# Performance work log

Hardware: AMD Instinct MI355X
Metric: run time of the kernel (lower is better)

Reference implementation:

```python
import jax, jax.numpy as jnp
import numpy as np

N = 12288
IN_DIM = 256
OUT_DIM = 128
NEG_SLOPE = 0.01  # torch nn.LeakyReLU default


def setup_inputs() -> dict:
    key = jax.random.key(0)
    k1, k2, k3, k4, k5 = jax.random.split(key, 5)
    adj_mx = jax.random.randint(k1, (N, N), 0, 2, dtype=jnp.int32)
    input_features = jax.random.normal(k2, (N, IN_DIM), dtype=jnp.float32)
    # Linear(in_dim, out_dim): weight [out, in], bias [out]
    W = jax.random.normal(k3, (OUT_DIM, IN_DIM), dtype=jnp.float32) / np.sqrt(IN_DIM)
    b = jax.random.normal(k4, (OUT_DIM,), dtype=jnp.float32) * 0.01
    phi = jax.random.normal(k5, (2 * OUT_DIM, 1), dtype=jnp.float32)
    return {"adj_mx": adj_mx, "input_features": input_features, "W": W, "b": b, "phi": phi}


def reference(adj_mx, input_features, W, b, phi):
    # projection (dropout is identity in eval): [N, out]
    new_features = input_features @ W.T + b
    # additive attention halves: (N,1) + (1,N) -> [N,N]
    first_half = new_features @ phi[:OUT_DIM]          # [N,1]
    second_half = (new_features @ phi[OUT_DIM:]).T     # [1,N]
    similarity = jax.nn.leaky_relu(first_half + second_half, NEG_SLOPE)
    # adjacency with self-loops; mask non-edges to -1e20
    adj_hat = adj_mx.astype(jnp.float32) + jnp.eye(adj_mx.shape[0], dtype=jnp.float32)
    masked = jnp.where(adj_hat > 0, similarity, jnp.float32(-1e20))
    att = jax.nn.softmax(masked, axis=1)               # row-wise softmax [N,N]
    out = att @ new_features                           # [N, out]
    return jax.nn.leaky_relu(out, NEG_SLOPE)
```

## Files before the change

kernel.cpp:

```cpp
#include <hip/hip_runtime.h>
#include <hip/hip_bf16.h>

#define N_NODES 12288
#define IN_DIM 256
#define OUT_DIM 128
#define NEG 0.01f
#define LOG2E 1.44269504088896340736f
#define NSPLIT 16
#define JSPAN (N_NODES / NSPLIT)
#define TJ 64
#define NT (JSPAN / TJ)

typedef __attribute__((ext_vector_type(8))) short short8;
typedef __attribute__((ext_vector_type(4))) float f32x4;
typedef __attribute__((ext_vector_type(4))) int i32x4;

__device__ __forceinline__ float fast_exp2(float x) {
#if __has_builtin(__builtin_amdgcn_exp2f)
  return __builtin_amdgcn_exp2f(x);
#else
  return exp2f(x);
#endif
}

__device__ __forceinline__ unsigned short f2bf(float x) {
  unsigned u = __float_as_uint(x);
  unsigned r = (u + 0x7FFFu + ((u >> 16) & 1u)) >> 16;
  return (unsigned short)r;
}

__global__ __launch_bounds__(256) void k1_proj(
    const float* __restrict__ X, const float* __restrict__ W,
    const float* __restrict__ bias, const float* __restrict__ phi,
    unsigned short* __restrict__ Vt, float* __restrict__ f,
    float* __restrict__ s, unsigned* __restrict__ smax) {
  __shared__ float Xs[32][40];
  __shared__ float Ws[32][136];
  __shared__ unsigned skey[8];
  const int t = threadIdx.x;
  const int i0 = blockIdx.x * 32;
  const int tx = t & 31, ty = t >> 5;
  float acc[4][4] = {};
  for (int k0 = 0; k0 < IN_DIM; k0 += 32) {
    __syncthreads();
    {
      int r = t >> 3, kq = (t & 7) * 4;
      float4 xv = *(const float4*)&X[(size_t)(i0 + r) * IN_DIM + k0 + kq];
      Xs[kq + 0][r] = xv.x; Xs[kq + 1][r] = xv.y;
      Xs[kq + 2][r] = xv.z; Xs[kq + 3][r] = xv.w;
    }
#pragma unroll
    for (int q = 0; q < 4; ++q) {
      int idx = t + q * 256;
      int c = idx >> 3, kq = (idx & 7) * 4;
      float4 wv = *(const float4*)&W[(size_t)c * IN_DIM + k0 + kq];
      Ws[kq + 0][c] = wv.x; Ws[kq + 1][c] = wv.y;
      Ws[kq + 2][c] = wv.z; Ws[kq + 3][c] = wv.w;
    }
    __syncthreads();
#pragma unroll
    for (int kk = 0; kk < 32; ++kk) {
      float4 a = *(const float4*)&Xs[kk][ty * 4];
      float4 bv = *(const float4*)&Ws[kk][tx * 4];
      float av[4] = {a.x, a.y, a.z, a.w};
      float bw[4] = {bv.x, bv.y, bv.z, bv.w};
#pragma unroll
      for (int r = 0; r < 4; ++r)
#pragma unroll
        for (int c = 0; c < 4; ++c) acc[r][c] += av[r] * bw[c];
    }
  }
  float4 bv = *(const float4*)&bias[tx * 4];
  float bb[4] = {bv.x, bv.y, bv.z, bv.w};
  float4 p1 = *(const float4*)&phi[tx * 4];
  float4 p2 = *(const float4*)&phi[OUT_DIM + tx * 4];
  float p1a[4] = {p1.x, p1.y, p1.z, p1.w};
  float p2a[4] = {p2.x, p2.y, p2.z, p2.w};
  float fp[4], sp_[4];
#pragma unroll
  for (int r = 0; r < 4; ++r) {
    int i = i0 + ty * 4 + r;
    float o[4];
    fp[r] = 0.f; sp_[r] = 0.f;
#pragma unroll
    for (int c = 0; c < 4; ++c) {
      o[c] = acc[r][c] + bb[c];
      Vt[(size_t)(tx * 4 + c) * N_NODES + i] = f2bf(o[c]);
      fp[r] = __builtin_fmaf(o[c], p1a[c], fp[r]);
      sp_[r] = __builtin_fmaf(o[c], p2a[c], sp_[r]);
    }
  }
#pragma unroll
  for (int o = 16; o; o >>= 1) {
#pragma unroll
    for (int r = 0; r < 4; ++r) {
      fp[r] += __shfl_xor(fp[r], o);
      sp_[r] += __shfl_xor(sp_[r], o);
    }
  }
  if (tx == 0) {
    unsigned kmax = 0;
#pragma unroll
    for (int r = 0; r < 4; ++r) {
      int i = i0 + ty * 4 + r;
      f[i] = fp[r]; s[i] = sp_[r];
      unsigned u = __float_as_uint(sp_[r]);
      unsigned key = (u & 0x80000000u) ? ~u : (u | 0x80000000u);
      kmax = max(kmax, key);
    }
    skey[ty] = kmax;
  }
  __syncthreads();
  if (t == 0) {
    unsigned kmax = skey[0];
#pragma unroll
    for (int q = 1; q < 8; ++q) kmax = max(kmax, skey[q]);
    atomicMax(smax, kmax);
  }
}

__global__ __launch_bounds__(256) void k3_attn(
    const int* __restrict__ adj, const unsigned short* __restrict__ Vt,
    const float* __restrict__ f, const float* __restrict__ s,
    const unsigned* __restrict__ smaxk,
    float* __restrict__ pacc, float* __restrict__ pden) {
  __shared__ float s_lds[JSPAN];
  __shared__ __align__(16) unsigned short vbuf[2][128 * TJ];
  const int t = threadIdx.x;
  const int sp = blockIdx.x & (NSPLIT - 1);
  const int rb = blockIdx.x >> 4;
  const int j0g = sp * JSPAN;
  const int w = t >> 6, l = t & 63;
  const int m = l & 15, slot = l >> 4;
  const int row_g = rb * 64 + w * 16 + m;
  if (t < JSPAN / 4) {
    *(float4*)&s_lds[t * 4] = *(const float4*)&s[j0g + t * 4];
  }
  unsigned key = *smaxk;
  unsigned ku = (key & 0x80000000u) ? (key ^ 0x80000000u) : ~key;
  const float smaxv = __uint_as_float(ku);
  const float fi = f[row_g];
  const float xm = fi + smaxv;
  const float mrow = fmaxf(xm, NEG * xm);
  const float em = mrow * LOG2E;
  const int diag_g = row_g - j0g;
  float dsum = 0.f;
  f32x4 acc[8] = {};
  const int* adjp = adj + (size_t)row_g * N_NODES + j0g + 8 * slot;
  const int srow = t >> 3, schunk = t & 7;
  const int xsw = schunk ^ (srow & 7);
  const unsigned short* vt_src = Vt + (size_t)srow * N_NODES + j0g + xsw * 8;
  const int off0 = m * TJ + ((slot) ^ (m & 7)) * 8;
  const int off1 = m * TJ + ((4 + slot) ^ (m & 7)) * 8;
  i32x4 aA[4], aB[4];

#define ADJ_LOAD(SET, TT) { int _o = (TT) * TJ;                       \
    SET[0] = *(const i32x4*)(adjp + _o);                              \
    SET[1] = *(const i32x4*)(adjp + _o + 4);                          \
    SET[2] = *(const i32x4*)(adjp + _o + 32);                         \
    SET[3] = *(const i32x4*)(adjp + _o + 36); }

#define STAGE(BB, TT) { const unsigned short* _s = vt_src + (TT) * TJ;      \
    unsigned short* _d = &vbuf[BB][t * 8];                                  \
    __builtin_amdgcn_global_load_lds(_s,                    _d,        16, 0, 0); \
    __builtin_amdgcn_global_load_lds(_s + 32 * N_NODES,     _d + 2048, 16, 0, 0); \
    __builtin_amdgcn_global_load_lds(_s + 64 * N_NODES,     _d + 4096, 16, 0, 0); \
    __builtin_amdgcn_global_load_lds(_s + 96 * N_NODES,     _d + 6144, 16, 0, 0); }

  STAGE(0, 0);
  ADJ_LOAD(aA, 0);
  ADJ_LOAD(aB, 1);

#define ITER(TT, SET) {                                                     \
    __syncthreads();      \
    STAGE(((TT) + 1) & 1, ((TT) + 1 < NT) ? (TT) + 1 : NT - 1);             \
    const unsigned short* rdp = &vbuf[(TT) & 1][0];                         \
    short8 b0[8], b1[8];                                                    \
    _Pragma("unroll")                                                       \
    for (int nt = 0; nt < 8; ++nt)                                          \
      b0[nt] = *(const short8*)(rdp + off0 + nt * 16 * TJ);                 \
    _Pragma("unroll")                                                       \
    for (int nt = 0; nt < 8; ++nt)                                          \
      b1[nt] = *(const short8*)(rdp + off1 + nt * 16 * TJ);                 \
    short8 af0, af1;                                                        \
    _Pragma("unroll")                                                       \
    for (int c = 0; c < 2; ++c) {                                           \
      int jb = (TT) * TJ + 32 * c + 8 * slot;                               \
      float4 sv0 = *(const float4*)&s_lds[jb];                              \
      float4 sv1 = *(const float4*)&s_lds[jb + 4];                          \
      int av[8] = {SET[2*c].x, SET[2*c].y, SET[2*c].z, SET[2*c].w,          \
                   SET[2*c+1].x, SET[2*c+1].y, SET[2*c+1].z, SET[2*c+1].w}; \
      float sva[8] = {sv0.x, sv0.y, sv0.z, sv0.w, sv1.x, sv1.y, sv1.z, sv1.w}; \
      _Pragma("unroll")                                                     \
      for (int q = 0; q < 8; ++q) {                                         \
        float x = fi + sva[q];                                              \
        float xl = fmaxf(x, NEG * x);                                       \
        float e = fast_exp2(__builtin_fmaf(xl, LOG2E, -em));                \
        bool edge = (av[q] > 0) || ((jb + q) == diag_g);                    \
        float p = edge ? e : 0.f;                                           \
        dsum += p;                                                          \
        if (c == 0) af0[q] = (short)f2bf(p); else af1[q] = (short)f2bf(p);  \
      }                                                                     \
    }                                                                       \
    ADJ_LOAD(SET, ((TT) + 2 < NT) ? (TT) + 2 : NT - 1);                     \
    _Pragma("unroll")                                                       \
    for (int nt = 0; nt < 8; ++nt)                                          \
      acc[nt] = __builtin_amdgcn_mfma_f32_16x16x32_bf16(af0, b0[nt], acc[nt], 0, 0, 0); \
    _Pragma("unroll")                                                       \
    for (int nt = 0; nt < 8; ++nt)                                          \
      acc[nt] = __builtin_amdgcn_mfma_f32_16x16x32_bf16(af1, b1[nt], acc[nt], 0, 0, 0); \
  }

  for (int tb = 0; tb < NT; tb += 2) {
    ITER(tb, aA);
    ITER(tb + 1, aB);
  }
#undef ITER
#undef STAGE
#undef ADJ_LOAD

  dsum += __shfl_xor(dsum, 16);
  dsum += __shfl_xor(dsum, 32);
  if (l < 16) pden[sp * N_NODES + rb * 64 + w * 16 + l] = dsum;
  float* pa = pacc + (size_t)sp * N_NODES * OUT_DIM;
#pragma unroll
  for (int nt = 0; nt < 8; ++nt)
#pragma unroll
    for (int r = 0; r < 4; ++r) {
      int ii = rb * 64 + w * 16 + slot * 4 + r;
      pa[(size_t)ii * OUT_DIM + nt * 16 + m] = acc[nt][r];
    }
}

__global__ __launch_bounds__(256) void k4_comb(
    const float* __restrict__ pacc, const float* __restrict__ pden,
    float* __restrict__ out) {
  int idx = blockIdx.x * 256 + threadIdx.x;
  int i = idx >> 7;
  float v = 0.f, den = 0.f;
#pragma unroll
  for (int spp = 0; spp < NSPLIT; ++spp) {
    v += pacc[(size_t)spp * N_NODES * OUT_DIM + idx];
    den += pden[spp * N_NODES + i];
  }
  float o = v / den;
  out[idx] = fmaxf(o, NEG * o);
}

extern "C" void kernel_launch(void* const* d_in, const int* in_sizes, int n_in,
                              void* d_out, int out_size, void* d_ws, size_t ws_size,
                              hipStream_t stream) {
  const int* adj = (const int*)d_in[0];
  const float* X = (const float*)d_in[1];
  const float* W = (const float*)d_in[2];
  const float* b = (const float*)d_in[3];
  const float* phi = (const float*)d_in[4];
  float* out = (float*)d_out;
  char* ws = (char*)d_ws;
  unsigned short* Vt = (unsigned short*)(ws);
  float* fv   = (float*)(ws + 3145728);
  float* sv   = (float*)(ws + 3194880);
  unsigned* smax = (unsigned*)(ws + 3244032);
  float* pden = (float*)(ws + 3244048);
  float* pacc = (float*)(ws + 4030480);

  hipMemsetAsync(smax, 0, 4, stream);
  hipLaunchKernelGGL(k1_proj, dim3(N_NODES / 32), dim3(256), 0, stream,
                     X, W, b, phi, Vt, fv, sv, smax);
  hipLaunchKernelGGL(k3_attn, dim3((N_NODES / 64) * NSPLIT), dim3(256), 0, stream,
                     adj, Vt, fv, sv, smax, pacc, pden);
  hipLaunchKernelGGL(k4_comb, dim3((N_NODES * OUT_DIM) / 256), dim3(256), 0, stream,
                     pacc, pden, out);
}
```

Baseline: 866.3 us.

## Stage adjacency tiles through LDS via async global-to-LDS loads and halve column splits

Adjacency values are no longer read into registers two tiles ahead. They are now copied asynchronously into a swizzled, double-buffered LDS tile with global_load_lds, alongside the V tile, and read back with XOR-swizzled offsets. The column split count drops from 16 to 8, which halves the partial-sum traffic and the combine work but gives half as many blocks. LDS use per block rises by 32KB, which may lower occupancy, and the final redundant prefetch is skipped.

```diff
diff --git a/kernel.cpp b/kernel.cpp
--- a/kernel.cpp
+++ b/kernel.cpp
@@ -6,7 +6,7 @@
 #define OUT_DIM 128
 #define NEG 0.01f
 #define LOG2E 1.44269504088896340736f
-#define NSPLIT 16
+#define NSPLIT 8
 #define JSPAN (N_NODES / NSPLIT)
 #define TJ 64
 #define NT (JSPAN / TJ)
@@ -126,15 +126,19 @@
     float* __restrict__ pacc, float* __restrict__ pden) {
   __shared__ float s_lds[JSPAN];
   __shared__ __align__(16) unsigned short vbuf[2][128 * TJ];
+  __shared__ __align__(16) int abuf[2][64 * TJ];
   const int t = threadIdx.x;
   const int sp = blockIdx.x & (NSPLIT - 1);
-  const int rb = blockIdx.x >> 4;
+  const int rb = blockIdx.x >> 3;
   const int j0g = sp * JSPAN;
   const int w = t >> 6, l = t & 63;
   const int m = l & 15, slot = l >> 4;
   const int row_g = rb * 64 + w * 16 + m;
-  if (t < JSPAN / 4) {
-    *(float4*)&s_lds[t * 4] = *(const float4*)&s[j0g + t * 4];
+#pragma unroll
+  for (int q = 0; q < 2; ++q) {
+    int idx = t + q * 256;
+    if (idx < JSPAN / 4)
+      *(float4*)&s_lds[idx * 4] = *(const float4*)&s[j0g + idx * 4];
   }
   unsigned key = *smaxk;
   unsigned ku = (key & 0x80000000u) ? (key ^ 0x80000000u) : ~key;
@@ -146,78 +150,81 @@
   const int diag_g = row_g - j0g;
   float dsum = 0.f;
   f32x4 acc[8] = {};
-  const int* adjp = adj + (size_t)row_g * N_NODES + j0g + 8 * slot;
   const int srow = t >> 3, schunk = t & 7;
   const int xsw = schunk ^ (srow & 7);
   const unsigned short* vt_src = Vt + (size_t)srow * N_NODES + j0g + xsw * 8;
   const int off0 = m * TJ + ((slot) ^ (m & 7)) * 8;
   const int off1 = m * TJ + ((4 + slot) ^ (m & 7)) * 8;
-  i32x4 aA[4], aB[4];
-
-#define ADJ_LOAD(SET, TT) { int _o = (TT) * TJ;                       \
-    SET[0] = *(const i32x4*)(adjp + _o);                              \
-    SET[1] = *(const i32x4*)(adjp + _o + 4);                          \
-    SET[2] = *(const i32x4*)(adjp + _o + 32);                         \
-    SET[3] = *(const i32x4*)(adjp + _o + 36); }
-
-#define STAGE(BB, TT) { const unsigned short* _s = vt_src + (TT) * TJ;      \
-    unsigned short* _d = &vbuf[BB][t * 8];                                  \
-    __builtin_amdgcn_global_load_lds(_s,                    _d,        16, 0, 0); \
-    __builtin_amdgcn_global_load_lds(_s + 32 * N_NODES,     _d + 2048, 16, 0, 0); \
-    __builtin_amdgcn_global_load_lds(_s + 64 * N_NODES,     _d + 4096, 16, 0, 0); \
-    __builtin_amdgcn_global_load_lds(_s + 96 * N_NODES,     _d + 6144, 16, 0, 0); }
+  const int arow = t >> 4, achk = t & 15;
+  const int* adj_src = adj + (size_t)(rb * 64 + arow) * N_NODES + j0g
+                       + ((achk ^ arow) * 4);
+  const int akk00 = ((2 * slot) ^ m) * 4,     akk01 = ((2 * slot + 1) ^ m) * 4;
+  const int akk10 = ((8 + 2 * slot) ^ m) * 4, akk11 = ((9 + 2 * slot) ^ m) * 4;
+
+#define STAGE(BB, TT) {                                                      \
+    const unsigned short* _vs = vt_src + (TT) * TJ;                          \
+    unsigned short* _vd = &vbuf[BB][t * 8];                                  \
+    __builtin_amdgcn_global_load_lds(_vs,                _vd,        16, 0, 0); \
+    __builtin_amdgcn_global_load_lds(_vs + 32 * N_NODES, _vd + 2048, 16, 0, 0); \
+    __builtin_amdgcn_global_load_lds(_vs + 64 * N_NODES, _vd + 4096, 16, 0, 0); \
+    __builtin_amdgcn_global_load_lds(_vs + 96 * N_NODES, _vd + 6144, 16, 0, 0); \
+    const int* _as = adj_src + (TT) * TJ;                                    \
+    int* _ad = &abuf[BB][arow * 64 + achk * 4];                              \
+    __builtin_amdgcn_global_load_lds(_as,                _ad,        16, 0, 0); \
+    __builtin_amdgcn_global_load_lds(_as + 16 * N_NODES, _ad + 1024, 16, 0, 0); \
+    __builtin_amdgcn_global_load_lds(_as + 32 * N_NODES, _ad + 2048, 16, 0, 0); \
+    __builtin_amdgcn_global_load_lds(_as + 48 * N_NODES, _ad + 3072, 16, 0, 0); }
 
   STAGE(0, 0);
-  ADJ_LOAD(aA, 0);
-  ADJ_LOAD(aB, 1);
-
-#define ITER(TT, SET) {                                                     \
-    __syncthreads();      \
-    STAGE(((TT) + 1) & 1, ((TT) + 1 < NT) ? (TT) + 1 : NT - 1);             \
-    const unsigned short* rdp = &vbuf[(TT) & 1][0];                         \
-    short8 b0[8], b1[8];                                                    \
-    _Pragma("unroll")                                                       \
-    for (int nt = 0; nt < 8; ++nt)                                          \
-      b0[nt] = *(const short8*)(rdp + off0 + nt * 16 * TJ);                 \
-    _Pragma("unroll")                                                       \
-    for (int nt = 0; nt < 8; ++nt)                                          \
-      b1[nt] = *(const short8*)(rdp + off1 + nt * 16 * TJ);                 \
-    short8 af0, af1;                                                        \
-    _Pragma("unroll")                                                       \
-    for (int c = 0; c < 2; ++c) {                                           \
-      int jb = (TT) * TJ + 32 * c + 8 * slot;                               \
-      float4 sv0 = *(const float4*)&s_lds[jb];                              \
-      float4 sv1 = *(const float4*)&s_lds[jb + 4];                          \
-      int av[8] = {SET[2*c].x, SET[2*c].y, SET[2*c].z, SET[2*c].w,          \
-                   SET[2*c+1].x, SET[2*c+1].y, SET[2*c+1].z, SET[2*c+1].w}; \
+
+#define ITER(TT) {                                                           \
+    __syncthreads();    \
+    if ((TT) + 1 < NT) STAGE(((TT) + 1) & 1, (TT) + 1);                      \
+    const unsigned short* rdp = &vbuf[(TT) & 1][0];                          \
+    const int* adp = &abuf[(TT) & 1][(w * 16 + m) * 64];     \
+    short8 b0[8], b1[8];                                                     \
+    _Pragma("unroll")                                                        \
+    for (int nt = 0; nt < 8; ++nt)                                           \
+      b0[nt] = *(const short8*)(rdp + off0 + nt * 16 * TJ);                  \
+    _Pragma("unroll")                                                        \
+    for (int nt = 0; nt < 8; ++nt)                                           \
+      b1[nt] = *(const short8*)(rdp + off1 + nt * 16 * TJ);                  \
+    i32x4 aq[4];                                                             \
+    aq[0] = *(const i32x4*)(adp + akk00); aq[1] = *(const i32x4*)(adp + akk01); \
+    aq[2] = *(const i32x4*)(adp + akk10); aq[3] = *(const i32x4*)(adp + akk11); \
+    short8 af0, af1;                                                         \
+    _Pragma("unroll")                                                        \
+    for (int c = 0; c < 2; ++c) {                                            \
+      int jb = (TT) * TJ + 32 * c + 8 * slot;                                \
+      float4 sv0 = *(const float4*)&s_lds[jb];                               \
+      float4 sv1 = *(const float4*)&s_lds[jb + 4];                           \
+      int av[8] = {aq[2*c].x, aq[2*c].y, aq[2*c].z, aq[2*c].w,               \
+                   aq[2*c+1].x, aq[2*c+1].y, aq[2*c+1].z, aq[2*c+1].w};      \
       float sva[8] = {sv0.x, sv0.y, sv0.z, sv0.w, sv1.x, sv1.y, sv1.z, sv1.w}; \
-      _Pragma("unroll")                                                     \
-      for (int q = 0; q < 8; ++q) {                                         \
-        float x = fi + sva[q];                                              \
-        float xl = fmaxf(x, NEG * x);                                       \
-        float e = fast_exp2(__builtin_fmaf(xl, LOG2E, -em));                \
-        bool edge = (av[q] > 0) || ((jb + q) == diag_g);                    \
-        float p = edge ? e : 0.f;                                           \
-        dsum += p;                                                          \
-        if (c == 0) af0[q] = (short)f2bf(p); else af1[q] = (short)f2bf(p);  \
-      }                                                                     \
-    }                                                                       \
-    ADJ_LOAD(SET, ((TT) + 2 < NT) ? (TT) + 2 : NT - 1);                     \
-    _Pragma("unroll")                                                       \
-    for (int nt = 0; nt < 8; ++nt)                                          \
+      _Pragma("unroll")                                                      \
+      for (int q = 0; q < 8; ++q) {                                          \
+        float x = fi + sva[q];                                               \
+        float xl = fmaxf(x, NEG * x);                                        \
+        float e = fast_exp2(__builtin_fmaf(xl, LOG2E, -em));                 \
+        bool edge = (av[q] > 0) || ((jb + q) == diag_g);                     \
+        float p = edge ? e : 0.f;                                            \
+        dsum += p;                                                           \
+        if (c == 0) af0[q] = (short)f2bf(p); else af1[q] = (short)f2bf(p);   \
+      }                                                                      \
+    }                                                                        \
+    _Pragma("unroll")                                                        \
+    for (int nt = 0; nt < 8; ++nt)                                           \
       acc[nt] = __builtin_amdgcn_mfma_f32_16x16x32_bf16(af0, b0[nt], acc[nt], 0, 0, 0); \
-    _Pragma("unroll")                                                       \
-    for (int nt = 0; nt < 8; ++nt)                                          \
+    _Pragma("unroll")                                                        \
+    for (int nt = 0; nt < 8; ++nt)                                           \
       acc[nt] = __builtin_amdgcn_mfma_f32_16x16x32_bf16(af1, b1[nt], acc[nt], 0, 0, 0); \
   }
 
-  for (int tb = 0; tb < NT; tb += 2) {
-    ITER(tb, aA);
-    ITER(tb + 1, aB);
+  for (int tb = 0; tb < NT; ++tb) {
+    ITER(tb);
   }
 #undef ITER
 #undef STAGE
-#undef ADJ_LOAD
 
   dsum += __shfl_xor(dsum, 16);
   dsum += __shfl_xor(dsum, 32);
@@ -262,7 +269,7 @@
   float* sv   = (float*)(ws + 3194880);
   unsigned* smax = (unsigned*)(ws + 3244032);
   float* pden = (float*)(ws + 3244048);
-  float* pacc = (float*)(ws + 4030480);
+  float* pacc = (float*)(ws + 3637264);
 
   hipMemsetAsync(smax, 0, 4, stream);
   hipLaunchKernelGGL(k1_proj, dim3(N_NODES / 32), dim3(256), 0, stream,
```

Result: no change. 853.5 us (-1.5%).
